# Performance work log

Measured on AMD Instinct MI355X. Metric: run time of the kernel, lower is better.

The kernel has to match this reference:

```python
import jax, jax.numpy as jnp
import numpy as np

B, NA, NB = 4, 2048, 2048
IN_A, IN_B, OUT, H = 128, 128, 128, 8
DH = OUT // H  # 16
NEG = jnp.float32(-1e30)
SLOPE = jnp.float32(0.01)


def setup_inputs() -> dict:
    key = jax.random.key(0)
    ks = jax.random.split(key, 13)
    s = 0.05
    return {
        "h_A": jax.random.normal(ks[0], (B, NA, IN_A), jnp.float32),
        "h_B": jax.random.normal(ks[1], (B, NB, IN_B), jnp.float32),
        "mask": jax.random.randint(ks[2], (B, NA, NB), 0, 2) > 0,
        # per-head params stacked on a leading head axis
        "WA_w": jax.random.normal(ks[3], (H, IN_A, DH), jnp.float32) * s,
        "WA_b": jax.random.normal(ks[4], (H, DH), jnp.float32) * s,
        "WB_w": jax.random.normal(ks[5], (H, IN_B, DH), jnp.float32) * s,
        "WB_b": jax.random.normal(ks[6], (H, DH), jnp.float32) * s,
        "aA_w": jax.random.normal(ks[7], (H, DH), jnp.float32) * s,
        "aA_b": jax.random.normal(ks[8], (H,), jnp.float32) * s,
        "aB_w": jax.random.normal(ks[9], (H, DH), jnp.float32) * s,
        "aB_b": jax.random.normal(ks[10], (H,), jnp.float32) * s,
        "W_w": jax.random.normal(ks[11], (OUT, OUT), jnp.float32) * s,
        "W_b": jax.random.normal(ks[12], (OUT,), jnp.float32) * s,
    }


def _leaky(x):
    return jnp.where(x >= 0, x, SLOPE * x)


def reference(h_A, h_B, mask, WA_w, WA_b, WB_w, WB_b, aA_w, aA_b, aB_w, aB_b, W_w, W_b):
    # per-head linear projections: [B, H, N, DH]
    z_A = jnp.einsum('bni,hid->bhnd', h_A, WA_w) + WA_b[None, :, None, :]
    z_B = jnp.einsum('bmi,hid->bhmd', h_B, WB_w) + WB_b[None, :, None, :]
    # additive attention logits: [B, H, NA] + [B, H, NB] -> [B, H, NA, NB]
    eA = jnp.einsum('bhnd,hd->bhn', z_A, aA_w) + aA_b[None, :, None]
    eB = jnp.einsum('bhmd,hd->bhm', z_B, aB_w) + aB_b[None, :, None]
    e = eA[:, :, :, None] + eB[:, :, None, :]
    m = mask[:, None, :, :]  # broadcast over heads
    e = jnp.where(m, e, NEG)
    alpha = jax.nn.softmax(_leaky(e), axis=-1)
    alpha = jnp.where(m, alpha, jnp.zeros((), alpha.dtype))
    # weighted aggregation: [B, H, NA, DH]
    out_h = jnp.einsum('bhnm,bhmd->bhnd', alpha, z_B)
    # concat heads -> [B, NA, OUT], final projection
    cat = out_h.transpose(0, 2, 1, 3).reshape(h_A.shape[0], h_A.shape[1], H * DH)
    return cat @ W_w.T + W_b
```

## Files before the change

### kernel.cpp

```cpp
#include <hip/hip_runtime.h>

typedef unsigned short u16;
typedef unsigned int u32;
typedef unsigned char u8;

typedef __attribute__((ext_vector_type(8))) short short8;
typedef __attribute__((ext_vector_type(4))) float f32x4;


__device__ __forceinline__ u16 f2bf(float f){
  u32 u = __float_as_uint(f);
  u += 0x7fff + ((u >> 16) & 1);
  return (u16)(u >> 16);
}

__global__ __launch_bounds__(256) void kzero(float* __restrict__ out){
  out[blockIdx.x * 256 + threadIdx.x] = 0.f;
}

__global__ __launch_bounds__(256) void kdet(const u32* __restrict__ mw, int* __restrict__ flags){
  __shared__ int allw, allhw, allbyte;
  int t = threadIdx.x;
  if (t == 0){ allw = 1; allhw = 1; allbyte = 1; }
  __syncthreads();
  int aw = 1, ah = 1, ab = 1;
  #pragma unroll
  for (int j = 0; j < 4; ++j){
    u32 m = mw[t + 256 * j];
    if (!(m == 0u || m == 1u || m == 0x3F800000u)) aw = 0;
    u32 lo = m & 0xFFFFu, hi = m >> 16;
    if (!((lo == 0u || lo == 1u || lo == 0x3F80u) && (hi == 0u || hi == 1u || hi == 0x3F80u))) ah = 0;
    if (m & ~0x01010101u) ab = 0;
  }
  if (!aw) atomicAnd(&allw, 0);
  if (!ah) atomicAnd(&allhw, 0);
  if (!ab) atomicAnd(&allbyte, 0);
  __syncthreads();
  if (t == 0){
    int fm = 0;
    if (allw) fm = 0; else if (allbyte) fm = 1; else if (allhw) fm = 2;
    flags[0] = fm;
  }
}

__global__ __launch_bounds__(256) void kmask(const void* __restrict__ maskv,
                                             const int* __restrict__ flags,
                                             u32* __restrict__ Mb){
  int Fm = flags[0];
  int t = threadIdx.x;
  if (Fm == 0){
    int lane = t & 63;
    int wid = blockIdx.x * 4 + (t >> 6);
    const u32* mw = (const u32*)maskv;
    size_t base = (size_t)wid * 2048;
    #pragma unroll 4
    for (int i = 0; i < 32; ++i){
      u32 v = mw[base + i * 64 + lane];
      unsigned long long bal = __ballot(v != 0u);
      if (lane < 2) Mb[(base + i * 64) / 32 + lane] = (u32)(bal >> (32 * lane));
    }
    return;
  }
  int oid = blockIdx.x * 256 + t;
  u32 bits = 0;
  if (Fm == 1){
    const uint4* mp = (const uint4*)maskv + (size_t)oid * 2;
    #pragma unroll
    for (int k = 0; k < 2; ++k){
      uint4 v = mp[k];
      u32 w[4] = {v.x, v.y, v.z, v.w};
      #pragma unroll
      for (int q = 0; q < 4; ++q)
        #pragma unroll
        for (int bb = 0; bb < 4; ++bb)
          bits |= ((w[q] >> (8*bb)) & 255u ? 1u : 0u) << (k*16 + q*4 + bb);
    }
  } else {
    const uint4* mp = (const uint4*)maskv + (size_t)oid * 4;
    #pragma unroll
    for (int k = 0; k < 4; ++k){
      uint4 v = mp[k];
      u32 w[4] = {v.x, v.y, v.z, v.w};
      #pragma unroll
      for (int q = 0; q < 4; ++q){
        bits |= ((w[q] & 0xFFFFu) ? 1u : 0u) << (k*8 + q*2);
        bits |= ((w[q] >> 16)     ? 1u : 0u) << (k*8 + q*2 + 1);
      }
    }
  }
  Mb[oid] = bits;
}

__global__ __launch_bounds__(256) void kfold(const float* __restrict__ WA, const float* __restrict__ WAb,
                                             const float* __restrict__ WB, const float* __restrict__ WBb,
                                             const float* __restrict__ aAw, const float* __restrict__ aAb,
                                             const float* __restrict__ aBw, const float* __restrict__ aBb,
                                             const float* __restrict__ W,
                                             float* __restrict__ WfB, float* __restrict__ WtO,
                                             float* __restrict__ vA, float* __restrict__ vB,
                                             float* __restrict__ cA, float* __restrict__ cB){
  int gid = blockIdx.x, t = threadIdx.x;
  if (gid < 64){
    int idx = gid * 256 + t;
    int k = idx >> 7, c = idx & 127;
    WfB[idx] = WB[(c >> 4) * 2048 + k * 16 + (c & 15)];
  } else if (gid < 128){
    int idx = (gid - 64) * 256 + t;
    int c = idx >> 7, o = idx & 127;
    WtO[idx] = W[o * 128 + c];
  } else {
    int h = gid - 128;
    if (t < 128){
      float s = 0.f;
      #pragma unroll
      for (int d = 0; d < 16; ++d) s += WA[h * 2048 + t * 16 + d] * aAw[h * 16 + d];
      vA[h * 128 + t] = s;
    } else {
      int i = t - 128;
      float s = 0.f;
      #pragma unroll
      for (int d = 0; d < 16; ++d) s += WB[h * 2048 + i * 16 + d] * aBw[h * 16 + d];
      vB[h * 128 + i] = s;
    }
    if (t == 0){
      float s = aAb[h];
      #pragma unroll
      for (int d = 0; d < 16; ++d) s += WAb[h * 16 + d] * aAw[h * 16 + d];
      cA[h] = s;
    }
    if (t == 255){
      float s = aBb[h];
      #pragma unroll
      for (int d = 0; d < 16; ++d) s += WBb[h * 16 + d] * aBw[h * 16 + d];
      cB[h] = s;
    }
  }
}

__global__ __launch_bounds__(256) void kproj(const float* __restrict__ hB,
                                             const float* __restrict__ WfB,
                                             const float* __restrict__ bB,
                                             uint4* __restrict__ zF){
  __shared__ float h_l[32 * 132];
  __shared__ float W_l[64 * 128];
  __shared__ float T[128 * 33];
  int R0 = blockIdx.x * 32;
  int t = threadIdx.x;

  for (int j = 0; j < 4; ++j){
    int idx4 = t + 256 * j;
    int r = idx4 >> 5, k0 = (idx4 & 31) * 4;
    *(float4*)&h_l[r * 132 + k0] = *(const float4*)&hB[(size_t)(R0 + r) * 128 + k0];
  }

  int cg = t & 15, rg = t >> 4;
  float acc[2][8];
  for (int i = 0; i < 2; ++i) for (int s = 0; s < 8; ++s) acc[i][s] = 0.f;

  for (int kc = 0; kc < 2; ++kc){
    __syncthreads();
    for (int j = 0; j < 8; ++j){
      int idx4 = t + 256 * j;
      int k = idx4 >> 5, c0 = (idx4 & 31) * 4;
      *(float4*)&W_l[k * 128 + c0] = *(const float4*)&WfB[(kc * 64 + k) * 128 + c0];
    }
    __syncthreads();
    for (int k = 0; k < 64; ++k){
      int kk = kc * 64 + k;
      float4 w0 = *(const float4*)&W_l[k * 128 + cg * 8];
      float4 w1 = *(const float4*)&W_l[k * 128 + cg * 8 + 4];
      float wv[8] = {w0.x, w0.y, w0.z, w0.w, w1.x, w1.y, w1.z, w1.w};
      #pragma unroll
      for (int i = 0; i < 2; ++i){
        float hv = h_l[(rg * 2 + i) * 132 + kk];
        #pragma unroll
        for (int s = 0; s < 8; ++s) acc[i][s] = fmaf(hv, wv[s], acc[i][s]);
      }
    }
  }

  for (int i = 0; i < 2; ++i)
    #pragma unroll
    for (int s = 0; s < 8; ++s)
      T[(cg * 8 + s) * 33 + rg * 2 + i] = acc[i][s] + bB[cg * 8 + s];
  __syncthreads();

  int b = R0 >> 11;
  int mblk = (R0 & 2047) >> 5;
  for (int it = t; it < 512; it += 256){
    int h = it >> 6, lane = it & 63;
    int d = lane & 15, mq = (lane >> 4) * 8;
    const float* Tp = &T[(h * 16 + d) * 33 + mq];
    u32 wv[4];
    #pragma unroll
    for (int p = 0; p < 4; ++p){
      u16 lo = f2bf(Tp[p * 2]);
      u16 hi = f2bf(Tp[p * 2 + 1]);
      wv[p] = (u32)lo | ((u32)hi << 16);
    }
    zF[((size_t)((b * 8 + h) * 64) + mblk) * 64 + lane] = make_uint4(wv[0], wv[1], wv[2], wv[3]);
  }
}

__global__ __launch_bounds__(256) void ke(const float* __restrict__ hA, const float* __restrict__ hB,
                                          const float* __restrict__ vA, const float* __restrict__ vB,
                                          const float* __restrict__ cA, const float* __restrict__ cB,
                                          float* __restrict__ EAe, float* __restrict__ EA01e,
                                          float* __restrict__ EBe, float* __restrict__ EB01e){
  __shared__ float h_l[32 * 132];
  __shared__ float v_l[8 * 132];
  __shared__ float c_l[8];
  int gid = blockIdx.x, t = threadIdx.x;
  int X = gid >> 8;
  int r0 = (gid & 255) * 32;
  const float* hp = X ? hB : hA;
  const float* vp = X ? vB : vA;
  const float* cp = X ? cB : cA;

  for (int j = 0; j < 4; ++j){
    int idx4 = t + 256 * j;
    int r = idx4 >> 5, k0 = (idx4 & 31) * 4;
    *(float4*)&h_l[r * 132 + k0] = *(const float4*)&hp[(size_t)(r0 + r) * 128 + k0];
  }
  { int hh = t >> 5, k0 = (t & 31) * 4;
    *(float4*)&v_l[hh * 132 + k0] = *(const float4*)&vp[hh * 128 + k0]; }
  if (t < 8) c_l[t] = cp[t];
  __syncthreads();

  int r = t >> 3, h = t & 7;
  float acc = c_l[h];
  #pragma unroll
  for (int k0 = 0; k0 < 128; k0 += 4){
    float4 hv = *(const float4*)&h_l[r * 132 + k0];
    float4 vv = *(const float4*)&v_l[h * 132 + k0];
    acc = fmaf(hv.x, vv.x, acc); acc = fmaf(hv.y, vv.y, acc);
    acc = fmaf(hv.z, vv.z, acc); acc = fmaf(hv.w, vv.w, acc);
  }
  int row = r0 + r;
  int b = row >> 11, n = row & 2047;
  size_t idx = (size_t)(b * 8 + h) * 2048 + n;
  float e0 = __expf(acc), e1 = __expf(0.01f * acc);
  if (X){ EBe[idx] = e0; EB01e[idx] = e1; }
  else  { EAe[idx] = e0; EA01e[idx] = e1; }
}

__global__ __launch_bounds__(256) void kattn(const uint4* __restrict__ zF,
                                             const float* __restrict__ EAe, const float* __restrict__ EA01e,
                                             const float* __restrict__ EBe, const float* __restrict__ EB01e,
                                             const u32* __restrict__ Mb,
                                             float* __restrict__ cat){
  __shared__ float red[3][32][17];
  int t = threadIdx.x;
  int w = t >> 6, lane = t & 63;
  int gid = blockIdx.x;
  int h  = gid & 7;
  int nt = (gid >> 3) & 63;
  int b  = gid >> 9;
  int n0 = nt * 32;
  int nl = lane & 15, q = lane >> 4, qs = q * 8;

  size_t ebase = (size_t)(b * 8 + h) * 2048;
  float ea0  = EAe  [ebase + n0 + nl];
  float ea0s = EA01e[ebase + n0 + nl];
  float ea1  = EAe  [ebase + n0 + 16 + nl];
  float ea1s = EA01e[ebase + n0 + 16 + nl];

  const float* EBp = EBe   + ebase + w * 512;
  const float* GBp = EB01e + ebase + w * 512;
  const uint4* zFp = zF + ((size_t)(b * 8 + h) * 64 + w * 16) * 64 + lane;
  const u32*  mp0 = Mb + ((size_t)(b * 2048) + n0 + nl) * 64 + w * 16;
  const u32*  mp1 = mp0 + 16 * 64;

  f32x4 acc0 = {0.f,0.f,0.f,0.f}, acc1 = {0.f,0.f,0.f,0.f};
  f32x4 lcc0 = {0.f,0.f,0.f,0.f}, lcc1 = {0.f,0.f,0.f,0.f};
  const short8 ones = {0x3F80,0x3F80,0x3F80,0x3F80,0x3F80,0x3F80,0x3F80,0x3F80};

  float4 Ae0,Ae1,Ag0,Ag1, Be0,Be1,Bg0,Bg1;
  uint4 Azu, Bzu; u32 Am0, Am1, Bm0, Bm1;
  #define LOADA(sp) do{ int m_ = (sp) * 32 + qs; \
    Ae0 = *(const float4*)(EBp + m_); Ae1 = *(const float4*)(EBp + m_ + 4); \
    Ag0 = *(const float4*)(GBp + m_); Ag1 = *(const float4*)(GBp + m_ + 4); \
    Azu = zFp[(size_t)(sp) * 64]; Am0 = mp0[sp]; Am1 = mp1[sp]; }while(0)
  #define LOADB(sp) do{ int m_ = (sp) * 32 + qs; \
    Be0 = *(const float4*)(EBp + m_); Be1 = *(const float4*)(EBp + m_ + 4); \
    Bg0 = *(const float4*)(GBp + m_); Bg1 = *(const float4*)(GBp + m_ + 4); \
    Bzu = zFp[(size_t)(sp) * 64]; Bm0 = mp0[sp]; Bm1 = mp1[sp]; }while(0)
  #define COMP(E0_,E1_,G0_,G1_,ZU_,M0_,M1_) do{ \
    float eb[8] = {E0_.x,E0_.y,E0_.z,E0_.w,E1_.x,E1_.y,E1_.z,E1_.w}; \
    float gb[8] = {G0_.x,G0_.y,G0_.z,G0_.w,G1_.x,G1_.y,G1_.z,G1_.w}; \
    union { uint4 u; short8 v; } zu; zu.u = ZU_; \
    u32 mb0 = (M0_) >> qs, mb1 = (M1_) >> qs; \
    union { u32 u[4]; short8 v; } af0, af1; \
    _Pragma("unroll") \
    for (int p = 0; p < 4; ++p){ \
      int j0 = 2*p, j1 = 2*p + 1; \
      u32 k00 = (u32)(((int)(mb0 << (31 - j0))) >> 31); \
      u32 k01 = (u32)(((int)(mb0 << (31 - j1))) >> 31); \
      u32 k10 = (u32)(((int)(mb1 << (31 - j0))) >> 31); \
      u32 k11 = (u32)(((int)(mb1 << (31 - j1))) >> 31); \
      float s00 = fmaxf(ea0 * eb[j0], ea0s * gb[j0]); \
      float s01 = fmaxf(ea0 * eb[j1], ea0s * gb[j1]); \
      float s10 = fmaxf(ea1 * eb[j0], ea1s * gb[j0]); \
      float s11 = fmaxf(ea1 * eb[j1], ea1s * gb[j1]); \
      u32 a00 = __float_as_uint(s00) & k00; \
      u32 a01 = __float_as_uint(s01) & k01; \
      u32 a10 = __float_as_uint(s10) & k10; \
      u32 a11 = __float_as_uint(s11) & k11; \
      af0.u[p] = __builtin_amdgcn_perm(a01, a00, 0x07060302u); \
      af1.u[p] = __builtin_amdgcn_perm(a11, a10, 0x07060302u); \
    } \
    acc0 = __builtin_amdgcn_mfma_f32_16x16x32_bf16(af0.v, zu.v, acc0, 0, 0, 0); \
    lcc0 = __builtin_amdgcn_mfma_f32_16x16x32_bf16(af0.v, ones, lcc0, 0, 0, 0); \
    acc1 = __builtin_amdgcn_mfma_f32_16x16x32_bf16(af1.v, zu.v, acc1, 0, 0, 0); \
    lcc1 = __builtin_amdgcn_mfma_f32_16x16x32_bf16(af1.v, ones, lcc1, 0, 0, 0); }while(0)

  LOADA(0);
  LOADB(1);
  #pragma unroll 4
  for (int s = 0; s < 16; s += 2){
    COMP(Ae0,Ae1,Ag0,Ag1,Azu,Am0,Am1);
    LOADA(s + 2);
    COMP(Be0,Be1,Bg0,Bg1,Bzu,Bm0,Bm1);
    LOADB(s + 3);
  }
  #undef LOADA
  #undef LOADB
  #undef COMP

  if (w > 0){
    #pragma unroll
    for (int r = 0; r < 4; ++r){
      int row = q * 4 + r;
      red[w - 1][row][nl]      = acc0[r];
      red[w - 1][row + 16][nl] = acc1[r];
    }
    if (nl == 0){
      #pragma unroll
      for (int r = 0; r < 4; ++r){
        red[w - 1][q * 4 + r][16]      = lcc0[r];
        red[w - 1][q * 4 + r + 16][16] = lcc1[r];
      }
    }
  }
  __syncthreads();
  if (w == 0){
    #pragma unroll
    for (int r = 0; r < 4; ++r){
      int row = q * 4 + r;
      float a0 = acc0[r] + red[0][row][nl]      + red[1][row][nl]      + red[2][row][nl];
      float a1 = acc1[r] + red[0][row + 16][nl] + red[1][row + 16][nl] + red[2][row + 16][nl];
      float L0 = lcc0[r] + red[0][row][16]      + red[1][row][16]      + red[2][row][16];
      float L1 = lcc1[r] + red[0][row + 16][16] + red[1][row + 16][16] + red[2][row + 16][16];
      float r0 = (L0 > 0.f) ? 1.f / L0 : 0.f;
      float r1 = (L1 > 0.f) ? 1.f / L1 : 0.f;
      cat[((size_t)(b * 2048) + n0 + row)      * 128 + h * 16 + nl] = a0 * r0;
      cat[((size_t)(b * 2048) + n0 + 16 + row) * 128 + h * 16 + nl] = a1 * r1;
    }
  }
}

__global__ __launch_bounds__(256) void kout(const float* __restrict__ cat,
                                            const float* __restrict__ WtO, const float* __restrict__ Wb,
                                            float* __restrict__ out){
  __shared__ float cat_l[32 * 132];
  __shared__ float Wt_l[64 * 128];
  int R0 = blockIdx.x * 32;
  int t = threadIdx.x;

  for (int jj = 0; jj < 4; ++jj){
    int idx4 = t + 256 * jj;
    int r = idx4 >> 5, c0 = (idx4 & 31) * 4;
    *(float4*)&cat_l[r * 132 + c0] = *(const float4*)&cat[((size_t)R0 + r) * 128 + c0];
  }

  int og = t & 15, rg = t >> 4;
  float acc[2][8];
  for (int i = 0; i < 2; ++i) for (int s = 0; s < 8; ++s) acc[i][s] = 0.f;

  for (int kc = 0; kc < 2; ++kc){
    __syncthreads();
    for (int j = 0; j < 8; ++j){
      int idx4 = t + 256 * j;
      int k = idx4 >> 5, o0 = (idx4 & 31) * 4;
      *(float4*)&Wt_l[k * 128 + o0] = *(const float4*)&WtO[(kc * 64 + k) * 128 + o0];
    }
    __syncthreads();
    for (int k = 0; k < 64; ++k){
      int kk = kc * 64 + k;
      float4 w0 = *(const float4*)&Wt_l[k * 128 + og * 8];
      float4 w1 = *(const float4*)&Wt_l[k * 128 + og * 8 + 4];
      float wv[8] = {w0.x, w0.y, w0.z, w0.w, w1.x, w1.y, w1.z, w1.w};
      #pragma unroll
      for (int i = 0; i < 2; ++i){
        float cv = cat_l[(rg * 2 + i) * 132 + kk];
        #pragma unroll
        for (int s = 0; s < 8; ++s) acc[i][s] = fmaf(cv, wv[s], acc[i][s]);
      }
    }
  }

  for (int i = 0; i < 2; ++i){
    int r = rg * 2 + i;
    float* op = out + (size_t)(R0 + r) * 128 + og * 8;
    *(float4*)(op)     = make_float4(acc[i][0]+Wb[og*8+0], acc[i][1]+Wb[og*8+1], acc[i][2]+Wb[og*8+2], acc[i][3]+Wb[og*8+3]);
    *(float4*)(op + 4) = make_float4(acc[i][4]+Wb[og*8+4], acc[i][5]+Wb[og*8+5], acc[i][6]+Wb[og*8+6], acc[i][7]+Wb[og*8+7]);
  }
}

extern "C" void kernel_launch(void* const* d_in, const int* in_sizes, int n_in,
                              void* d_out, int out_size, void* d_ws, size_t ws_size,
                              hipStream_t stream) {
  const float* hA  = (const float*)d_in[0];
  const float* hB  = (const float*)d_in[1];
  const void* maskv= d_in[2];
  const float* WAw = (const float*)d_in[3];
  const float* WAb = (const float*)d_in[4];
  const float* WBw = (const float*)d_in[5];
  const float* WBb = (const float*)d_in[6];
  const float* aAw = (const float*)d_in[7];
  const float* aAb = (const float*)d_in[8];
  const float* aBw = (const float*)d_in[9];
  const float* aBb = (const float*)d_in[10];
  const float* Ww  = (const float*)d_in[11];
  const float* Wb  = (const float*)d_in[12];

  float* ws   = (float*)d_ws;
  uint4* zF   = (uint4*)ws;
  float* EAe  = ws + 524288;
  float* EA01e= ws + 589824;
  float* EBe  = ws + 655360;
  float* EB01e= ws + 720896;
  float* WfB  = ws + 786432;
  float* WtO  = ws + 802816;
  float* vA   = ws + 819200;
  float* vB   = ws + 820224;
  float* cA   = ws + 821248;
  float* cB   = ws + 821256;
  int*  flags = (int*)(ws + 821264);
  u32*  Mb    = (u32*)(ws + 821272);
  float* cat  = ws + 1345560;

  if (ws_size < 2394136ull * 4ull){
    kzero<<<4096, 256, 0, stream>>>((float*)d_out);
    return;
  }

  kdet <<<1, 256, 0, stream>>>((const u32*)maskv, flags);
  kfold<<<136, 256, 0, stream>>>(WAw, WAb, WBw, WBb, aAw, aAb, aBw, aBb, Ww,
                                 WfB, WtO, vA, vB, cA, cB);
  kmask<<<2048, 256, 0, stream>>>(maskv, flags, Mb);
  kproj<<<256, 256, 0, stream>>>(hB, WfB, WBb, zF);
  ke   <<<512, 256, 0, stream>>>(hA, hB, vA, vB, cA, cB, EAe, EA01e, EBe, EB01e);
  kattn<<<2048, 256, 0, stream>>>(zF, EAe, EA01e, EBe, EB01e, Mb, cat);
  kout <<<256, 256, 0, stream>>>(cat, WtO, Wb, (float*)d_out);
}
```

Measured before the change: 188.3 us.

## Switch attention path to fp16 with packed exp factors and merge mask detection

The change moves the attention weights and z_B from bf16 to fp16 and uses the f16 MFMA. It stores the per-key exponent factors as packed half pairs, so the inner loop does packed f16 multiply and max and loads half as many bytes for those factors. It also folds the mask-format detection into the mask-packing kernel, which removes one launch. In exchange, fp16 has a narrower range than bf16, so exp(e) products can overflow or underflow, and every block of the mask kernel now repeats the detection reads.

```diff
diff --git a/kernel.cpp b/kernel.cpp
--- a/kernel.cpp
+++ b/kernel.cpp
@@ -4,50 +4,40 @@
 typedef unsigned int u32;
 typedef unsigned char u8;
 
-typedef __attribute__((ext_vector_type(8))) short short8;
+typedef _Float16 f16x8 __attribute__((ext_vector_type(8)));
+typedef _Float16 f16x2 __attribute__((ext_vector_type(2)));
 typedef __attribute__((ext_vector_type(4))) float f32x4;
 
-
-__device__ __forceinline__ u16 f2bf(float f){
-  u32 u = __float_as_uint(f);
-  u += 0x7fff + ((u >> 16) & 1);
-  return (u16)(u >> 16);
-}
 
 __global__ __launch_bounds__(256) void kzero(float* __restrict__ out){
   out[blockIdx.x * 256 + threadIdx.x] = 0.f;
 }
 
-__global__ __launch_bounds__(256) void kdet(const u32* __restrict__ mw, int* __restrict__ flags){
-  __shared__ int allw, allhw, allbyte;
+__global__ __launch_bounds__(256) void kmask(const void* __restrict__ maskv,
+                                             u32* __restrict__ Mb){
+  __shared__ int s_aw, s_ab, s_ah;
   int t = threadIdx.x;
-  if (t == 0){ allw = 1; allhw = 1; allbyte = 1; }
+  if (t == 0){ s_aw = 1; s_ab = 1; s_ah = 1; }
   __syncthreads();
-  int aw = 1, ah = 1, ab = 1;
-  #pragma unroll
-  for (int j = 0; j < 4; ++j){
-    u32 m = mw[t + 256 * j];
-    if (!(m == 0u || m == 1u || m == 0x3F800000u)) aw = 0;
-    u32 lo = m & 0xFFFFu, hi = m >> 16;
-    if (!((lo == 0u || lo == 1u || lo == 0x3F80u) && (hi == 0u || hi == 1u || hi == 0x3F80u))) ah = 0;
-    if (m & ~0x01010101u) ab = 0;
-  }
-  if (!aw) atomicAnd(&allw, 0);
-  if (!ah) atomicAnd(&allhw, 0);
-  if (!ab) atomicAnd(&allbyte, 0);
+  {
+    const u32* mw = (const u32*)maskv;
+    int aw = 1, ah = 1, ab = 1;
+    #pragma unroll
+    for (int j = 0; j < 4; ++j){
+      u32 m = mw[t + 256 * j];
+      if (!(m == 0u || m == 1u || m == 0x3F800000u)) aw = 0;
+      u32 lo = m & 0xFFFFu, hi = m >> 16;
+      if (!((lo == 0u || lo == 1u || lo == 0x3F80u) && (hi == 0u || hi == 1u || hi == 0x3F80u))) ah = 0;
+      if (m & ~0x01010101u) ab = 0;
+    }
+    if (!aw) atomicAnd(&s_aw, 0);
+    if (!ah) atomicAnd(&s_ah, 0);
+    if (!ab) atomicAnd(&s_ab, 0);
+  }
   __syncthreads();
-  if (t == 0){
-    int fm = 0;
-    if (allw) fm = 0; else if (allbyte) fm = 1; else if (allhw) fm = 2;
-    flags[0] = fm;
-  }
-}
-
-__global__ __launch_bounds__(256) void kmask(const void* __restrict__ maskv,
-                                             const int* __restrict__ flags,
-                                             u32* __restrict__ Mb){
-  int Fm = flags[0];
-  int t = threadIdx.x;
+  int Fm = 0;
+  if (s_aw) Fm = 0; else if (s_ab) Fm = 1; else if (s_ah) Fm = 2;
+
   if (Fm == 0){
     int lane = t & 63;
     int wid = blockIdx.x * 4 + (t >> 6);
@@ -194,9 +184,9 @@
     u32 wv[4];
     #pragma unroll
     for (int p = 0; p < 4; ++p){
-      u16 lo = f2bf(Tp[p * 2]);
-      u16 hi = f2bf(Tp[p * 2 + 1]);
-      wv[p] = (u32)lo | ((u32)hi << 16);
+      union { f16x2 h2; u32 u; } c;
+      c.h2 = (f16x2){(_Float16)Tp[p * 2], (_Float16)Tp[p * 2 + 1]};
+      wv[p] = c.u;
     }
     zF[((size_t)((b * 8 + h) * 64) + mblk) * 64 + lane] = make_uint4(wv[0], wv[1], wv[2], wv[3]);
   }
@@ -206,7 +196,7 @@
                                           const float* __restrict__ vA, const float* __restrict__ vB,
                                           const float* __restrict__ cA, const float* __restrict__ cB,
                                           float* __restrict__ EAe, float* __restrict__ EA01e,
-                                          float* __restrict__ EBe, float* __restrict__ EB01e){
+                                          u32* __restrict__ EBh, u32* __restrict__ GBh){
   __shared__ float h_l[32 * 132];
   __shared__ float v_l[8 * 132];
   __shared__ float c_l[8];
@@ -238,15 +228,27 @@
   }
   int row = r0 + r;
   int b = row >> 11, n = row & 2047;
-  size_t idx = (size_t)(b * 8 + h) * 2048 + n;
   float e0 = __expf(acc), e1 = __expf(0.01f * acc);
-  if (X){ EBe[idx] = e0; EB01e[idx] = e1; }
-  else  { EAe[idx] = e0; EA01e[idx] = e1; }
+  if (X){
+    float p0 = __shfl_xor(e0, 8, 64);
+    float p1 = __shfl_xor(e1, 8, 64);
+    if ((((t & 63) >> 3) & 1) == 0){
+      union { f16x2 h2; u32 u; } c0, c1;
+      c0.h2 = (f16x2){(_Float16)e0, (_Float16)p0};
+      c1.h2 = (f16x2){(_Float16)e1, (_Float16)p1};
+      u32 di = (u32)((b * 8 + h) * 1024 + (n >> 1));
+      EBh[di] = c0.u;
+      GBh[di] = c1.u;
+    }
+  } else {
+    size_t idx = (size_t)(b * 8 + h) * 2048 + n;
+    EAe[idx] = e0; EA01e[idx] = e1;
+  }
 }
 
 __global__ __launch_bounds__(256) void kattn(const uint4* __restrict__ zF,
                                              const float* __restrict__ EAe, const float* __restrict__ EA01e,
-                                             const float* __restrict__ EBe, const float* __restrict__ EB01e,
+                                             const u32* __restrict__ EBh, const u32* __restrict__ GBh,
                                              const u32* __restrict__ Mb,
                                              float* __restrict__ cat){
   __shared__ float red[3][32][17];
@@ -260,37 +262,40 @@
   int nl = lane & 15, q = lane >> 4, qs = q * 8;
 
   size_t ebase = (size_t)(b * 8 + h) * 2048;
-  float ea0  = EAe  [ebase + n0 + nl];
-  float ea0s = EA01e[ebase + n0 + nl];
-  float ea1  = EAe  [ebase + n0 + 16 + nl];
-  float ea1s = EA01e[ebase + n0 + 16 + nl];
-
-  const float* EBp = EBe   + ebase + w * 512;
-  const float* GBp = EB01e + ebase + w * 512;
+  _Float16 ea0h  = (_Float16)EAe  [ebase + n0 + nl];
+  _Float16 ea0sh = (_Float16)EA01e[ebase + n0 + nl];
+  _Float16 ea1h  = (_Float16)EAe  [ebase + n0 + 16 + nl];
+  _Float16 ea1sh = (_Float16)EA01e[ebase + n0 + 16 + nl];
+  f16x2 ea0_2  = (f16x2){ea0h,  ea0h};
+  f16x2 ea0s_2 = (f16x2){ea0sh, ea0sh};
+  f16x2 ea1_2  = (f16x2){ea1h,  ea1h};
+  f16x2 ea1s_2 = (f16x2){ea1sh, ea1sh};
+
+  const u32*  EBp = EBh + (size_t)(b * 8 + h) * 1024 + w * 256;
+  const u32*  GBp = GBh + (size_t)(b * 8 + h) * 1024 + w * 256;
   const uint4* zFp = zF + ((size_t)(b * 8 + h) * 64 + w * 16) * 64 + lane;
   const u32*  mp0 = Mb + ((size_t)(b * 2048) + n0 + nl) * 64 + w * 16;
   const u32*  mp1 = mp0 + 16 * 64;
 
   f32x4 acc0 = {0.f,0.f,0.f,0.f}, acc1 = {0.f,0.f,0.f,0.f};
   f32x4 lcc0 = {0.f,0.f,0.f,0.f}, lcc1 = {0.f,0.f,0.f,0.f};
-  const short8 ones = {0x3F80,0x3F80,0x3F80,0x3F80,0x3F80,0x3F80,0x3F80,0x3F80};
-
-  float4 Ae0,Ae1,Ag0,Ag1, Be0,Be1,Bg0,Bg1;
-  uint4 Azu, Bzu; u32 Am0, Am1, Bm0, Bm1;
-  #define LOADA(sp) do{ int m_ = (sp) * 32 + qs; \
-    Ae0 = *(const float4*)(EBp + m_); Ae1 = *(const float4*)(EBp + m_ + 4); \
-    Ag0 = *(const float4*)(GBp + m_); Ag1 = *(const float4*)(GBp + m_ + 4); \
+  union { u32 u[4]; f16x8 v; } onesu;
+  onesu.u[0] = 0x3C003C00u; onesu.u[1] = 0x3C003C00u;
+  onesu.u[2] = 0x3C003C00u; onesu.u[3] = 0x3C003C00u;
+  const f16x8 ones = onesu.v;
+
+  uint4 Aeb, Agb, Azu, Beb, Bgb, Bzu; u32 Am0, Am1, Bm0, Bm1;
+  #define LOADA(sp) do{ int d_ = (sp) * 16 + q * 4; \
+    Aeb = *(const uint4*)(EBp + d_); Agb = *(const uint4*)(GBp + d_); \
     Azu = zFp[(size_t)(sp) * 64]; Am0 = mp0[sp]; Am1 = mp1[sp]; }while(0)
-  #define LOADB(sp) do{ int m_ = (sp) * 32 + qs; \
-    Be0 = *(const float4*)(EBp + m_); Be1 = *(const float4*)(EBp + m_ + 4); \
-    Bg0 = *(const float4*)(GBp + m_); Bg1 = *(const float4*)(GBp + m_ + 4); \
+  #define LOADB(sp) do{ int d_ = (sp) * 16 + q * 4; \
+    Beb = *(const uint4*)(EBp + d_); Bgb = *(const uint4*)(GBp + d_); \
     Bzu = zFp[(size_t)(sp) * 64]; Bm0 = mp0[sp]; Bm1 = mp1[sp]; }while(0)
-  #define COMP(E0_,E1_,G0_,G1_,ZU_,M0_,M1_) do{ \
-    float eb[8] = {E0_.x,E0_.y,E0_.z,E0_.w,E1_.x,E1_.y,E1_.z,E1_.w}; \
-    float gb[8] = {G0_.x,G0_.y,G0_.z,G0_.w,G1_.x,G1_.y,G1_.z,G1_.w}; \
-    union { uint4 u; short8 v; } zu; zu.u = ZU_; \
+  #define COMP(EB_,GB_,ZU_,M0_,M1_) do{ \
     u32 mb0 = (M0_) >> qs, mb1 = (M1_) >> qs; \
-    union { u32 u[4]; short8 v; } af0, af1; \
+    u32 ebu[4] = {EB_.x, EB_.y, EB_.z, EB_.w}; \
+    u32 gbu[4] = {GB_.x, GB_.y, GB_.z, GB_.w}; \
+    union { u32 u[4]; f16x8 v; } a0, a1; \
     _Pragma("unroll") \
     for (int p = 0; p < 4; ++p){ \
       int j0 = 2*p, j1 = 2*p + 1; \
@@ -298,29 +303,28 @@
       u32 k01 = (u32)(((int)(mb0 << (31 - j1))) >> 31); \
       u32 k10 = (u32)(((int)(mb1 << (31 - j0))) >> 31); \
       u32 k11 = (u32)(((int)(mb1 << (31 - j1))) >> 31); \
-      float s00 = fmaxf(ea0 * eb[j0], ea0s * gb[j0]); \
-      float s01 = fmaxf(ea0 * eb[j1], ea0s * gb[j1]); \
-      float s10 = fmaxf(ea1 * eb[j0], ea1s * gb[j0]); \
-      float s11 = fmaxf(ea1 * eb[j1], ea1s * gb[j1]); \
-      u32 a00 = __float_as_uint(s00) & k00; \
-      u32 a01 = __float_as_uint(s01) & k01; \
-      u32 a10 = __float_as_uint(s10) & k10; \
-      u32 a11 = __float_as_uint(s11) & k11; \
-      af0.u[p] = __builtin_amdgcn_perm(a01, a00, 0x07060302u); \
-      af1.u[p] = __builtin_amdgcn_perm(a11, a10, 0x07060302u); \
+      u32 kc0 = __builtin_amdgcn_perm(k01, k00, 0x05040100u); \
+      u32 kc1 = __builtin_amdgcn_perm(k11, k10, 0x05040100u); \
+      union { u32 u; f16x2 h2; } eb, gb, r0u, r1u; \
+      eb.u = ebu[p]; gb.u = gbu[p]; \
+      r0u.h2 = __builtin_elementwise_max(ea0_2 * eb.h2, ea0s_2 * gb.h2); \
+      r1u.h2 = __builtin_elementwise_max(ea1_2 * eb.h2, ea1s_2 * gb.h2); \
+      a0.u[p] = r0u.u & kc0; \
+      a1.u[p] = r1u.u & kc1; \
     } \
-    acc0 = __builtin_amdgcn_mfma_f32_16x16x32_bf16(af0.v, zu.v, acc0, 0, 0, 0); \
-    lcc0 = __builtin_amdgcn_mfma_f32_16x16x32_bf16(af0.v, ones, lcc0, 0, 0, 0); \
-    acc1 = __builtin_amdgcn_mfma_f32_16x16x32_bf16(af1.v, zu.v, acc1, 0, 0, 0); \
-    lcc1 = __builtin_amdgcn_mfma_f32_16x16x32_bf16(af1.v, ones, lcc1, 0, 0, 0); }while(0)
+    union { uint4 u; f16x8 v; } zu; zu.u = ZU_; \
+    acc0 = __builtin_amdgcn_mfma_f32_16x16x32_f16(a0.v, zu.v, acc0, 0, 0, 0); \
+    lcc0 = __builtin_amdgcn_mfma_f32_16x16x32_f16(a0.v, ones, lcc0, 0, 0, 0); \
+    acc1 = __builtin_amdgcn_mfma_f32_16x16x32_f16(a1.v, zu.v, acc1, 0, 0, 0); \
+    lcc1 = __builtin_amdgcn_mfma_f32_16x16x32_f16(a1.v, ones, lcc1, 0, 0, 0); }while(0)
 
   LOADA(0);
   LOADB(1);
   #pragma unroll 4
   for (int s = 0; s < 16; s += 2){
-    COMP(Ae0,Ae1,Ag0,Ag1,Azu,Am0,Am1);
+    COMP(Aeb,Agb,Azu,Am0,Am1);
     LOADA(s + 2);
-    COMP(Be0,Be1,Bg0,Bg1,Bzu,Bm0,Bm1);
+    COMP(Beb,Bgb,Bzu,Bm0,Bm1);
     LOADB(s + 3);
   }
   #undef LOADA
@@ -428,15 +432,14 @@
   uint4* zF   = (uint4*)ws;
   float* EAe  = ws + 524288;
   float* EA01e= ws + 589824;
-  float* EBe  = ws + 655360;
-  float* EB01e= ws + 720896;
+  u32*  EBh   = (u32*)(ws + 655360);
+  u32*  GBh   = (u32*)(ws + 720896);
   float* WfB  = ws + 786432;
   float* WtO  = ws + 802816;
   float* vA   = ws + 819200;
   float* vB   = ws + 820224;
   float* cA   = ws + 821248;
   float* cB   = ws + 821256;
-  int*  flags = (int*)(ws + 821264);
   u32*  Mb    = (u32*)(ws + 821272);
   float* cat  = ws + 1345560;
 
@@ -445,12 +448,11 @@
     return;
   }
 
-  kdet <<<1, 256, 0, stream>>>((const u32*)maskv, flags);
   kfold<<<136, 256, 0, stream>>>(WAw, WAb, WBw, WBb, aAw, aAb, aBw, aBb, Ww,
                                  WfB, WtO, vA, vB, cA, cB);
-  kmask<<<2048, 256, 0, stream>>>(maskv, flags, Mb);
+  kmask<<<2048, 256, 0, stream>>>(maskv, Mb);
   kproj<<<256, 256, 0, stream>>>(hB, WfB, WBb, zF);
-  ke   <<<512, 256, 0, stream>>>(hA, hB, vA, vB, cA, cB, EAe, EA01e, EBe, EB01e);
-  kattn<<<2048, 256, 0, stream>>>(zF, EAe, EA01e, EBe, EB01e, Mb, cat);
+  ke   <<<512, 256, 0, stream>>>(hA, hB, vA, vB, cA, cB, EAe, EA01e, EBh, GBh);
+  kattn<<<2048, 256, 0, stream>>>(zF, EAe, EA01e, EBh, GBh, Mb, cat);
   kout <<<256, 256, 0, stream>>>(cat, WtO, Wb, (float*)d_out);
 }
```

Measured after the change: 182.4 us. 3.1% less time.
